# Performance work log

Hardware: AMD Instinct MI355X
Metric: run time of the kernel (lower is better)

The kernel has to match this reference:

```python
import jax, jax.numpy as jnp
import numpy as np

B, N = 4, 2466  # batch, vertex count (Pixel2Mesh stage-3 mesh)
IMG = 224.0


def _vertex_align(feat_maps, pos):
    """Bilinear-style gather of image features at projected vertex locations.
    feat_maps: list of [B,C,S,S]; pos: [B,N,3]. Returns [B,N,sum(C)]."""
    z = pos[..., 2]
    h = jnp.clip(248.0 * (pos[..., 1] / z) + 111.5, 0.0, 223.0)
    w = jnp.clip(248.0 * (pos[..., 0] / (-z)) + 111.5, 0.0, 223.0)
    outs = []
    for f in feat_maps:
        S = f.shape[-1]
        x = h / (IMG / S)
        y = w / (IMG / S)
        x1 = jnp.floor(x).astype(jnp.int32)
        x2 = jnp.minimum(jnp.ceil(x).astype(jnp.int32), S - 1)
        y1 = jnp.floor(y).astype(jnp.int32)
        y2 = jnp.minimum(jnp.ceil(y).astype(jnp.int32), S - 1)
        xi = x.astype(jnp.int32)  # trunc == floor since x >= 0
        yi = y.astype(jnp.int32)

        def gat(fm, xs, ys):  # fm [C,S,S], xs/ys [N] -> [N,C]
            return fm[:, xs, ys].T

        g = jax.vmap(gat)
        w11 = ((x2 - xi) * (y2 - yi)).astype(f.dtype)[..., None]
        w12 = ((x2 - xi) * (yi - y1)).astype(f.dtype)[..., None]
        w21 = ((xi - x1) * (y2 - yi)).astype(f.dtype)[..., None]
        w22 = ((xi - x1) * (yi - y1)).astype(f.dtype)[..., None]
        outs.append(w11 * g(f, x1, y1) + w21 * g(f, x2, y1)
                    + w12 * g(f, x1, y2) + w22 * g(f, x2, y2))
    return jnp.concatenate(outs, axis=-1)


def _graph_conv(x, adj, w0, w1):
    # relu(X @ w0 + A @ (X @ w1))
    return jax.nn.relu(x @ w0 + jnp.einsum('bmn,bnc->bmc', adj, x @ w1))


def _res_graph_conv(x, adj, pw, pb, w00, w01, w10, w11):
    skip = x @ pw + pb
    out = _graph_conv(x, adj, w00, w01)
    out = _graph_conv(out, adj, w10, w11)
    return skip + out


def _forward(conv2_3, conv3_4, conv4_6, conv5_3, vertex_positions, vertex_features,
             vertex_adjacency, lin_w, lin_b,
             r0_pw, r0_pb, r0_w00, r0_w01, r0_w10, r0_w11,
             r1_pw, r1_pb, r1_w00, r1_w01, r1_w10, r1_w11,
             r2_pw, r2_pb, r2_w00, r2_w01, r2_w10, r2_w11,
             gf_w0, gf_w1):
    aligned = _vertex_align([conv2_3, conv3_4, conv4_6, conv5_3], vertex_positions)  # [B,N,3840]
    proj = aligned @ lin_w + lin_b  # [B,N,128]
    x = jnp.concatenate([proj, vertex_features, vertex_positions], axis=-1)  # [B,N,259]
    x = _res_graph_conv(x, vertex_adjacency, r0_pw, r0_pb, r0_w00, r0_w01, r0_w10, r0_w11)
    x = _res_graph_conv(x, vertex_adjacency, r1_pw, r1_pb, r1_w00, r1_w01, r1_w10, r1_w11)
    x = _res_graph_conv(x, vertex_adjacency, r2_pw, r2_pb, r2_w00, r2_w01, r2_w10, r2_w11)
    offset = jnp.tanh(_graph_conv(x, vertex_adjacency, gf_w0, gf_w1))  # [B,N,3]
    return vertex_positions + offset


def setup_inputs() -> dict:
    key = jax.random.key(0)
    ks = jax.random.split(key, 40)
    inp = {
        "conv2_3": jax.random.normal(ks[0], (B, 256, 56, 56), jnp.float32),
        "conv3_4": jax.random.normal(ks[1], (B, 512, 28, 28), jnp.float32),
        "conv4_6": jax.random.normal(ks[2], (B, 1024, 14, 14), jnp.float32),
        "conv5_3": jax.random.normal(ks[3], (B, 2048, 7, 7), jnp.float32),
        "vertex_positions": jax.random.normal(ks[4], (B, N, 3), jnp.float32),
        "vertex_features": jax.random.normal(ks[5], (B, N, 128), jnp.float32),
        # sparse 0/1 adjacency stored dense (the torch module uses dense bmm)
        "vertex_adjacency": (jax.random.uniform(ks[6], (B, N, N)) < 0.003).astype(jnp.float32),
    }

    def u(k, shape, fan):
        b = 1.0 / np.sqrt(fan)
        return jax.random.uniform(k, shape, jnp.float32, -b, b)

    specs = [("lin_w", (3840, 128), 3840), ("lin_b", (128,), 3840)]
    for j, ci in enumerate([259, 128, 128]):
        p = f"r{j}_"
        specs += [(p + "pw", (ci, 128), ci), (p + "pb", (128,), ci),
                  (p + "w00", (ci, 128), ci), (p + "w01", (ci, 128), ci),
                  (p + "w10", (128, 128), 128), (p + "w11", (128, 128), 128)]
    specs += [("gf_w0", (128, 3), 128), ("gf_w1", (128, 3), 128)]
    for i, (name, shape, fan) in enumerate(specs):
        inp[name] = u(ks[7 + i], shape, fan)
    return inp


def reference(conv2_3, conv3_4, conv4_6, conv5_3, vertex_positions, vertex_features,
              vertex_adjacency, lin_w, lin_b,
              r0_pw, r0_pb, r0_w00, r0_w01, r0_w10, r0_w11,
              r1_pw, r1_pb, r1_w00, r1_w01, r1_w10, r1_w11,
              r2_pw, r2_pb, r2_w00, r2_w01, r2_w10, r2_w11,
              gf_w0, gf_w1):
    return _forward(conv2_3, conv3_4, conv4_6, conv5_3, vertex_positions, vertex_features,
                    vertex_adjacency, lin_w, lin_b,
                    r0_pw, r0_pb, r0_w00, r0_w01, r0_w10, r0_w11,
                    r1_pw, r1_pb, r1_w00, r1_w01, r1_w10, r1_w11,
                    r2_pw, r2_pb, r2_w00, r2_w01, r2_w10, r2_w11,
                    gf_w0, gf_w1)
```

## Files before the change

kernel.cpp:

```cpp
#include <hip/hip_runtime.h>
#include <cmath>

#define B_   4
#define N_   2466
#define R_   (B_*N_)
#define ELLW 96

typedef _Float16 f16x8 __attribute__((ext_vector_type(8)));
typedef _Float16 f16x4 __attribute__((ext_vector_type(4)));
typedef __attribute__((ext_vector_type(4))) float f32x4;

__device__ __forceinline__ unsigned short f16_bits(float x) {
  union { _Float16 h; unsigned short u; } c;
  c.h = (_Float16)x;
  return c.u;
}

struct WMats { const float* p[15]; };


__global__ __launch_bounds__(256) void k_pre(
    const float* __restrict__ c2, const float* __restrict__ c3,
    const float* __restrict__ c4, const float* __restrict__ c5,
    unsigned short* __restrict__ t0, unsigned short* __restrict__ t1,
    unsigned short* __restrict__ t2, unsigned short* __restrict__ t3,
    const float* __restrict__ adj, int* __restrict__ cols, int* __restrict__ cnts,
    const float* __restrict__ lin_w,
    unsigned short* __restrict__ whf,
    WMats wm,
    unsigned short* __restrict__ wrf) {
  __shared__ float t[64][66];
  int bid = blockIdx.x;
  int tid = threadIdx.x;
  if (bid < 1584) {
    const float* in; unsigned short* out; int C, P, npb, ncb, rem;
    if (bid < 784)       { in = c2; out = t0; C = 256;  P = 3136; npb = 49; ncb = 4;  rem = bid; }
    else if (bid < 1200) { in = c3; out = t1; C = 512;  P = 784;  npb = 13; ncb = 8;  rem = bid - 784; }
    else if (bid < 1456) { in = c4; out = t2; C = 1024; P = 196;  npb = 4;  ncb = 16; rem = bid - 1200; }
    else                 { in = c5; out = t3; C = 2048; P = 49;   npb = 1;  ncb = 32; rem = bid - 1456; }
    int pb = rem % npb; int tq = rem / npb; int cb = tq % ncb; int b = tq / ncb;
    int c0 = cb * 64, p0 = pb * 64;
    #pragma unroll
    for (int i = 0; i < 8; i++) {
      int e = tid + i * 256;
      int c = e >> 5, f2 = e & 31;
      int p = p0 + f2 * 2;
      float2 v = make_float2(0.f, 0.f);
      const float* src = in + ((size_t)b * C + (c0 + c)) * P + p;
      if (p + 1 < P)      v = *(const float2*)src;
      else if (p < P)     v.x = *src;
      *(float2*)&t[c][f2 * 2] = v;
    }
    __syncthreads();
    int jj = tid & 15, c4i = jj * 4;
    #pragma unroll
    for (int pass = 0; pass < 4; pass++) {
      int pp = pass * 16 + (tid >> 4);
      int px = p0 + pp;
      if (px < P) {
        ushort4 o;
        o.x = f16_bits(t[c4i + 0][pp]);
        o.y = f16_bits(t[c4i + 1][pp]);
        o.z = f16_bits(t[c4i + 2][pp]);
        o.w = f16_bits(t[c4i + 3][pp]);
        *(ushort4*)&out[((size_t)b * P + px) * C + c0 + c4i] = o;
      }
    }
  } else if (bid < 4050) {
    int wave = tid >> 6, lane = tid & 63;
    int row = (bid - 1584) * 4 + wave;
    const float* Ar = adj + (size_t)row * N_;
    int* cp = cols + (size_t)row * ELLW;
    unsigned long long below = (lane == 63) ? 0xFFFFFFFFFFFFFFFFull >> 1
                                            : ((1ull << lane) - 1ull);
    float4 v[10];
    #pragma unroll
    for (int i0 = 0; i0 < 10; i0++) {
      int j0 = i0 * 256 + lane * 4;
      if (j0 + 3 < N_) {
        v[i0] = *(const float4*)&Ar[j0];
      } else {
        v[i0] = make_float4(0.f, 0.f, 0.f, 0.f);
        if (j0     < N_) v[i0].x = Ar[j0];
        if (j0 + 1 < N_) v[i0].y = Ar[j0+1];
        if (j0 + 2 < N_) v[i0].z = Ar[j0+2];
      }
    }
    int base = 0;
    #pragma unroll
    for (int i0 = 0; i0 < 10; i0++) {
      int j0 = i0 * 256 + lane * 4;
      bool nz0 = (j0     < N_) && (v[i0].x != 0.f);
      bool nz1 = (j0 + 1 < N_) && (v[i0].y != 0.f);
      bool nz2 = (j0 + 2 < N_) && (v[i0].z != 0.f);
      bool nz3 = (j0 + 3 < N_) && (v[i0].w != 0.f);
      unsigned long long m0 = __ballot(nz0);
      unsigned long long m1 = __ballot(nz1);
      unsigned long long m2 = __ballot(nz2);
      unsigned long long m3 = __ballot(nz3);
      int pre = __popcll(m0 & below) + __popcll(m1 & below)
              + __popcll(m2 & below) + __popcll(m3 & below);
      int p0 = base + pre;
      int p1 = p0 + (nz0 ? 1 : 0);
      int p2 = p1 + (nz1 ? 1 : 0);
      int p3 = p2 + (nz2 ? 1 : 0);
      if (nz0 && p0 < ELLW) cp[p0] = j0;
      if (nz1 && p1 < ELLW) cp[p1] = j0 + 1;
      if (nz2 && p2 < ELLW) cp[p2] = j0 + 2;
      if (nz3 && p3 < ELLW) cp[p3] = j0 + 3;
      base += __popcll(m0) + __popcll(m1) + __popcll(m2) + __popcll(m3);
    }
    if (lane == 0) cnts[row] = (base > ELLW) ? ELLW : base;
  } else if (bid < 4530) {
    int b = bid - 4050;
    int e0 = (b * 256 + tid) * 4;
    #pragma unroll
    for (int u = 0; u < 4; u++) {
      int e = e0 + u;
      int j = e & 7;
      int lane = (e >> 3) & 63;
      int nt = (e >> 9) & 7;
      int slab = e >> 12;
      int k = slab * 32 + ((lane >> 4) << 3) + j;
      int n = nt * 16 + (lane & 15);
      whf[e] = f16_bits(lin_w[(size_t)k * 128 + n]);
    }
  } else {
    int b = bid - 4530;
    int e0 = (b * 256 + tid) * 4;
    #pragma unroll
    for (int u = 0; u < 4; u++) {
      int e = e0 + u;
      int rb, mat, rem, K;
      if (e < 143360) {
        rb = 0;
        if (e < 110592) { mat = e / 36864; rem = e - mat * 36864; K = 259; }
        else { int tt = e - 110592; mat = 3 + tt / 16384; rem = tt & 16383; K = 128; }
      } else {
        int tt = e - 143360;
        rb = 1 + tt / 81920;
        int r2 = tt % 81920;
        mat = r2 / 16384; rem = r2 & 16383; K = 128;
      }
      int j = rem & 7, lane = (rem >> 3) & 63, nt = (rem >> 9) & 7, slab = rem >> 12;
      int k = slab * 32 + ((lane >> 4) << 3) + j;
      int n = nt * 16 + (lane & 15);
      float x = (k < K) ? wm.p[rb * 5 + mat][(size_t)k * 128 + n] : 0.f;
      wrf[e] = f16_bits(x);
    }
  }
}

__global__ __launch_bounds__(256) void k_align_mfma(
    const unsigned short* __restrict__ tr0, const unsigned short* __restrict__ tr1,
    const unsigned short* __restrict__ tr2, const unsigned short* __restrict__ tr3,
    const float* __restrict__ pos,
    const unsigned short* __restrict__ whf,
    unsigned short* __restrict__ part, int kchunk) {
  int tid  = threadIdx.x;
  int wave = tid >> 6, lane = tid & 63;
  int q    = lane >> 4, l15 = lane & 15;
  int m0   = blockIdx.x * 128;
  int s    = blockIdx.y;

  int zero[2][4]; int base[2][4];
  #pragma unroll
  for (int u = 0; u < 2; u++) {
    int mrow = m0 + (wave * 2 + u) * 16 + l15;
    int rowc = (mrow < R_) ? mrow : 0;
    int b = rowc / N_;
    float px = pos[rowc*3+0], py = pos[rowc*3+1], pz = pos[rowc*3+2];
    float hh = fminf(fmaxf(248.f*(py/pz)    + 111.5f, 0.f), 223.f);
    float wc = fminf(fmaxf(248.f*(px/(-pz)) + 111.5f, 0.f), 223.f);
    const int Sarr[4] = {56, 28, 14, 7};
    const int Carr[4] = {256, 512, 1024, 2048};
    #pragma unroll
    for (int sc = 0; sc < 4; sc++) {
      int S = Sarr[sc], C = Carr[sc];
      float dv = 224.f / (float)S;
      float x = hh / dv, y = wc / dv;
      int x1 = (int)floorf(x), y1 = (int)floorf(y);
      int x2 = min((int)ceilf(x), S - 1), y2 = min((int)ceilf(y), S - 1);
      int w = (x2 - x1) * (y2 - y1);
      zero[u][sc] = (mrow >= R_) || (w == 0);
      base[u][sc] = (b * S * S + x1 * S + y1) * C;
    }
  }

  f32x4 acc[2][8];
  #pragma unroll
  for (int u = 0; u < 2; u++)
    #pragma unroll
    for (int nt = 0; nt < 8; nt++) acc[u][nt] = (f32x4){0.f, 0.f, 0.f, 0.f};

  const f16x8* BH = (const f16x8*)whf;

  int kbeg = s * kchunk, kend = kbeg + kchunk;
  #pragma unroll 1
  for (int k0 = kbeg; k0 < kend; k0 += 32) {
    const unsigned short* tr; int off, sI;
    if (k0 < 256)       { tr = tr0; off = 0;    sI = 0; }
    else if (k0 < 768)  { tr = tr1; off = 256;  sI = 1; }
    else if (k0 < 1792) { tr = tr2; off = 768;  sI = 2; }
    else                { tr = tr3; off = 1792; sI = 3; }

    f16x8 af[2];
    #pragma unroll
    for (int u = 0; u < 2; u++) {
      af[u] = *(const f16x8*)(tr + base[u][sI] + (k0 - off) + q * 8);
      if (zero[u][sI]) af[u] = (f16x8)(_Float16)0;
    }

    int slab = k0 >> 5;
    f16x8 Bh[8];
    #pragma unroll
    for (int nt = 0; nt < 8; nt++)
      Bh[nt] = BH[(size_t)(slab * 8 + nt) * 64 + lane];
    #pragma unroll
    for (int nt = 0; nt < 8; nt++) {
      acc[0][nt] = __builtin_amdgcn_mfma_f32_16x16x32_f16(af[0], Bh[nt], acc[0][nt], 0, 0, 0);
      acc[1][nt] = __builtin_amdgcn_mfma_f32_16x16x32_f16(af[1], Bh[nt], acc[1][nt], 0, 0, 0);
    }
  }

  #pragma unroll
  for (int u = 0; u < 2; u++)
    #pragma unroll
    for (int nt = 0; nt < 8; nt++)
      #pragma unroll
      for (int r = 0; r < 4; r++) {
        int row = m0 + (wave * 2 + u) * 16 + q * 4 + r;
        if (row < R_)
          part[((size_t)s * R_ + row) * 128 + nt * 16 + l15] = f16_bits(acc[u][nt][r]);
      }
}

__global__ __launch_bounds__(256) void k_reduce(
    const unsigned short* __restrict__ part, const float* __restrict__ lin_b,
    const float* __restrict__ vf, const float* __restrict__ pos,
    unsigned short* __restrict__ xcat, int nsplit) {
  int grp = threadIdx.x >> 5, ln = threadIdx.x & 31;
  int row = blockIdx.x * 8 + grp;
  float4 acc = ((const float4*)lin_b)[ln];
  const f16x4* p4 = (const f16x4*)part;
  for (int s = 0; s < nsplit; s++) {
    f16x4 pv = p4[((size_t)s * R_ + row) * 32 + ln];
    acc.x += (float)pv[0]; acc.y += (float)pv[1];
    acc.z += (float)pv[2]; acc.w += (float)pv[3];
  }
  ushort4* xr = (ushort4*)(xcat + (size_t)row * 288);
  ushort4 o;
  o.x = f16_bits(acc.x); o.y = f16_bits(acc.y);
  o.z = f16_bits(acc.z); o.w = f16_bits(acc.w);
  xr[ln] = o;
  float4 vv = ((const float4*)vf)[(size_t)row * 32 + ln];
  o.x = f16_bits(vv.x); o.y = f16_bits(vv.y);
  o.z = f16_bits(vv.z); o.w = f16_bits(vv.w);
  xr[32 + ln] = o;
  if (ln < 8) {
    ushort4 z = make_ushort4(0, 0, 0, 0);
    if (ln == 0) {
      z.x = f16_bits(pos[(size_t)row * 3 + 0]);
      z.y = f16_bits(pos[(size_t)row * 3 + 1]);
      z.z = f16_bits(pos[(size_t)row * 3 + 2]);
    }
    xr[64 + ln] = z;
  }
}

template<int SLABS>
__global__ __launch_bounds__(256) void k_gemm_mfma(
    const unsigned short* __restrict__ X, int ldx,
    const unsigned short* __restrict__ wf,
    int matStride, const float* __restrict__ pb,
    unsigned short* __restrict__ o0, unsigned short* __restrict__ o1,
    unsigned short* __restrict__ o2) {
  int tid = threadIdx.x;
  int wave = tid >> 6, lane = tid & 63;
  int q = lane >> 4, l15 = lane & 15;
  int which = blockIdx.y;
  int m0 = blockIdx.x * 64;
  int mrow = m0 + wave * 16 + l15;
  int rowc = (mrow < R_) ? mrow : (R_ - 1);
  const unsigned short* xrow = X + (size_t)rowc * ldx + q * 8;

  const f16x8* BH = (const f16x8*)(wf + (size_t)which * matStride);

  f32x4 acc[8];
  #pragma unroll
  for (int nt = 0; nt < 8; nt++) acc[nt] = (f32x4){0.f, 0.f, 0.f, 0.f};

  #pragma unroll 1
  for (int slab = 0; slab < SLABS; slab++) {
    f16x8 af = *(const f16x8*)(xrow + slab * 32);
    f16x8 Bh[8];
    #pragma unroll
    for (int nt = 0; nt < 8; nt++)
      Bh[nt] = BH[(size_t)(slab * 8 + nt) * 64 + lane];
    #pragma unroll
    for (int nt = 0; nt < 8; nt++)
      acc[nt] = __builtin_amdgcn_mfma_f32_16x16x32_f16(af, Bh[nt], acc[nt], 0, 0, 0);
  }

  unsigned short* out = (which == 0) ? o0 : (which == 1) ? o1 : o2;
  #pragma unroll
  for (int nt = 0; nt < 8; nt++) {
    int col = nt * 16 + l15;
    float bias = (pb != nullptr && which == 2) ? pb[col] : 0.f;
    #pragma unroll
    for (int r = 0; r < 4; r++) {
      int row = m0 + wave * 16 + q * 4 + r;
      if (row < R_) out[(size_t)row * 128 + col] = f16_bits(acc[nt][r] + bias);
    }
  }
}

template<int NW>
__global__ __launch_bounds__(256) void k_fuse(
    const unsigned short* __restrict__ s_in,
    const unsigned short* __restrict__ t_in,
    const unsigned short* __restrict__ skip_in,
    const int* __restrict__ cols, const int* __restrict__ cnts,
    const unsigned short* __restrict__ wf, const float* __restrict__ pb,
    unsigned short* __restrict__ o0, unsigned short* __restrict__ o1,
    unsigned short* __restrict__ o2) {
  __shared__ unsigned short hsm[32][136];
  int tid = threadIdx.x;
  int r0 = blockIdx.x * 32;

  {
    int grp = tid >> 5, ln = tid & 31;
    const f16x4* s4 = (const f16x4*)s_in;
    const f16x4* t4 = (const f16x4*)t_in;
    #pragma unroll 1
    for (int rr = 0; rr < 4; rr++) {
      int lrow = grp * 4 + rr;
      int row = r0 + lrow;
      int rowc = (row < R_) ? row : (R_ - 1);
      int b = rowc / N_;
      size_t tbase = (size_t)b * N_;
      const int* cp = cols + (size_t)rowc * ELLW;
      int4 ci0 = *(const int4*)cp;
      int4 ci1 = *(const int4*)(cp + 4);
      int4 ci2 = *(const int4*)(cp + 8);
      int cnt = cnts[rowc];
      f16x4 sv = s4[(size_t)rowc*32 + ln];
      float4 acc = make_float4((float)sv[0], (float)sv[1], (float)sv[2], (float)sv[3]);
      int idx[12] = {ci0.x, ci0.y, ci0.z, ci0.w, ci1.x, ci1.y, ci1.z, ci1.w,
                     ci2.x, ci2.y, ci2.z, ci2.w};
      f16x4 g[12];
      #pragma unroll
      for (int i = 0; i < 12; i++) {
        int c = idx[i];
        c = (c >= 0 && c < N_) ? c : 0;
        g[i] = t4[(tbase + c)*32 + ln];
      }
      #pragma unroll
      for (int i = 0; i < 12; i++) {
        if (i < cnt) {
          acc.x += (float)g[i][0]; acc.y += (float)g[i][1];
          acc.z += (float)g[i][2]; acc.w += (float)g[i][3];
        }
      }
      for (int i = 12; i < cnt; i++) {
        f16x4 v = t4[(tbase + cp[i])*32 + ln];
        acc.x += (float)v[0]; acc.y += (float)v[1];
        acc.z += (float)v[2]; acc.w += (float)v[3];
      }
      acc.x = fmaxf(acc.x, 0.f); acc.y = fmaxf(acc.y, 0.f);
      acc.z = fmaxf(acc.z, 0.f); acc.w = fmaxf(acc.w, 0.f);
      if (skip_in) {
        f16x4 sk = ((const f16x4*)skip_in)[(size_t)rowc*32 + ln];
        acc.x += (float)sk[0]; acc.y += (float)sk[1];
        acc.z += (float)sk[2]; acc.w += (float)sk[3];
      }
      ushort4 o;
      o.x = f16_bits(acc.x); o.y = f16_bits(acc.y);
      o.z = f16_bits(acc.z); o.w = f16_bits(acc.w);
      *(ushort4*)&hsm[lrow][ln * 4] = o;
    }
  }
  __syncthreads();

  int wave = tid >> 6, lane = tid & 63;
  int q = lane >> 4, l15 = lane & 15;
  int mt = wave & 1, nh = wave >> 1;
  const unsigned short* xrow = &hsm[mt * 16 + l15][q * 8];

  #pragma unroll 1
  for (int which = 0; which < NW; which++) {
    const f16x8* BH = (const f16x8*)(wf + (size_t)which * 16384);
    f32x4 acc[4];
    #pragma unroll
    for (int t2 = 0; t2 < 4; t2++) acc[t2] = (f32x4){0.f, 0.f, 0.f, 0.f};
    #pragma unroll
    for (int slab = 0; slab < 4; slab++) {
      f16x8 af = *(const f16x8*)(xrow + slab * 32);
      f16x8 Bh[4];
      #pragma unroll
      for (int t2 = 0; t2 < 4; t2++)
        Bh[t2] = BH[(size_t)(slab * 8 + nh * 4 + t2) * 64 + lane];
      #pragma unroll
      for (int t2 = 0; t2 < 4; t2++)
        acc[t2] = __builtin_amdgcn_mfma_f32_16x16x32_f16(af, Bh[t2], acc[t2], 0, 0, 0);
    }
    unsigned short* out = (which == 0) ? o0 : (which == 1) ? o1 : o2;
    #pragma unroll
    for (int t2 = 0; t2 < 4; t2++) {
      int col = (nh * 4 + t2) * 16 + l15;
      float bias = (pb != nullptr && which == 2) ? pb[col] : 0.f;
      #pragma unroll
      for (int r = 0; r < 4; r++) {
        int row = r0 + mt * 16 + q * 4 + r;
        if (row < R_) out[(size_t)row * 128 + col] = f16_bits(acc[t2][r] + bias);
      }
    }
  }
}

__global__ __launch_bounds__(256) void k_spmm(
    const unsigned short* __restrict__ sb, const unsigned short* __restrict__ tb,
    const int* __restrict__ cols, const int* __restrict__ cnts,
    const unsigned short* __restrict__ skipb, unsigned short* __restrict__ outb,
    const float* __restrict__ gw0, const float* __restrict__ gw1,
    unsigned short* __restrict__ gsb, unsigned short* __restrict__ gtb, int fuse_gf) {
  int tid = threadIdx.x;
  int grp = tid >> 5, ln = tid & 31;
  int row = blockIdx.x * 8 + grp;
  int b = row / N_;
  size_t tbase = (size_t)b * N_;
  const f16x4* sb4 = (const f16x4*)sb;
  const f16x4* tb4 = (const f16x4*)tb;
  const int* cp = cols + (size_t)row * ELLW;
  int4 ci0 = *(const int4*)cp;
  int4 ci1 = *(const int4*)(cp + 4);
  int4 ci2 = *(const int4*)(cp + 8);
  int cnt = cnts[row];
  f16x4 sv = sb4[(size_t)row*32 + ln];
  float4 acc = make_float4((float)sv[0], (float)sv[1], (float)sv[2], (float)sv[3]);
  int idx[12] = {ci0.x, ci0.y, ci0.z, ci0.w, ci1.x, ci1.y, ci1.z, ci1.w,
                 ci2.x, ci2.y, ci2.z, ci2.w};
  f16x4 g[12];
  #pragma unroll
  for (int i = 0; i < 12; i++) {
    int c = idx[i];
    c = (c >= 0 && c < N_) ? c : 0;
    g[i] = tb4[(tbase + c)*32 + ln];
  }
  #pragma unroll
  for (int i = 0; i < 12; i++) {
    if (i < cnt) {
      acc.x += (float)g[i][0]; acc.y += (float)g[i][1];
      acc.z += (float)g[i][2]; acc.w += (float)g[i][3];
    }
  }
  for (int i = 12; i < cnt; i++) {
    f16x4 v = tb4[(tbase + cp[i])*32 + ln];
    acc.x += (float)v[0]; acc.y += (float)v[1];
    acc.z += (float)v[2]; acc.w += (float)v[3];
  }
  acc.x = fmaxf(acc.x, 0.f); acc.y = fmaxf(acc.y, 0.f);
  acc.z = fmaxf(acc.z, 0.f); acc.w = fmaxf(acc.w, 0.f);
  if (skipb) {
    f16x4 sk = ((const f16x4*)skipb)[(size_t)row*32 + ln];
    acc.x += (float)sk[0]; acc.y += (float)sk[1];
    acc.z += (float)sk[2]; acc.w += (float)sk[3];
  }
  if (!fuse_gf) {
    ushort4 o;
    o.x = f16_bits(acc.x); o.y = f16_bits(acc.y);
    o.z = f16_bits(acc.z); o.w = f16_bits(acc.w);
    ((ushort4*)outb)[(size_t)row*32 + ln] = o;
    return;
  }
  float av[4] = {acc.x, acc.y, acc.z, acc.w};
  int j0 = ln * 4;
  float p0 = 0.f, p1 = 0.f, p2 = 0.f, q0 = 0.f, q1 = 0.f, q2 = 0.f;
  #pragma unroll
  for (int u = 0; u < 4; u++) {
    int j = j0 + u;
    p0 += av[u] * gw0[j*3+0]; p1 += av[u] * gw0[j*3+1]; p2 += av[u] * gw0[j*3+2];
    q0 += av[u] * gw1[j*3+0]; q1 += av[u] * gw1[j*3+1]; q2 += av[u] * gw1[j*3+2];
  }
  #pragma unroll
  for (int off = 16; off >= 1; off >>= 1) {
    p0 += __shfl_xor(p0, off); p1 += __shfl_xor(p1, off); p2 += __shfl_xor(p2, off);
    q0 += __shfl_xor(q0, off); q1 += __shfl_xor(q1, off); q2 += __shfl_xor(q2, off);
  }
  if (ln == 0) {
    gsb[(size_t)row*128 + 0] = f16_bits(p0);
    gsb[(size_t)row*128 + 1] = f16_bits(p1);
    gsb[(size_t)row*128 + 2] = f16_bits(p2);
    gtb[(size_t)row*128 + 0] = f16_bits(q0);
    gtb[(size_t)row*128 + 1] = f16_bits(q1);
    gtb[(size_t)row*128 + 2] = f16_bits(q2);
  }
}

__global__ __launch_bounds__(256) void k_gf_final(
    const unsigned short* __restrict__ sb, const unsigned short* __restrict__ tb,
    const int* __restrict__ cols, const int* __restrict__ cnts,
    const float* __restrict__ pos, float* __restrict__ out) {
  int wave = threadIdx.x >> 6, lane = threadIdx.x & 63;
  int row = blockIdx.x * 4 + wave;
  if (lane >= 3) return;
  int b = row / N_;
  size_t tbase = (size_t)b * N_;
  const int* cp = cols + (size_t)row * ELLW;
  int4 ci0 = *(const int4*)cp;
  int4 ci1 = *(const int4*)(cp + 4);
  int4 ci2 = *(const int4*)(cp + 8);
  int cnt = cnts[row];
  union { unsigned short u; _Float16 h; } cv;
  cv.u = sb[(size_t)row*128 + lane];
  float acc = (float)cv.h;
  int idx[12] = {ci0.x, ci0.y, ci0.z, ci0.w, ci1.x, ci1.y, ci1.z, ci1.w,
                 ci2.x, ci2.y, ci2.z, ci2.w};
  float g[12];
  #pragma unroll
  for (int i = 0; i < 12; i++) {
    int c = idx[i];
    c = (c >= 0 && c < N_) ? c : 0;
    cv.u = tb[(tbase + c)*128 + lane];
    g[i] = (float)cv.h;
  }
  #pragma unroll
  for (int i = 0; i < 12; i++)
    if (i < cnt) acc += g[i];
  for (int i = 12; i < cnt; i++) {
    cv.u = tb[(tbase + cp[i])*128 + lane];
    acc += (float)cv.h;
  }
  float v = tanhf(fmaxf(acc, 0.f));
  out[(size_t)row*3 + lane] = pos[(size_t)row*3 + lane] + v;
}

extern "C" void kernel_launch(void* const* d_in, const int* in_sizes, int n_in,
                              void* d_out, int out_size, void* d_ws, size_t ws_size,
                              hipStream_t stream) {
  const float* conv2_3 = (const float*)d_in[0];
  const float* conv3_4 = (const float*)d_in[1];
  const float* conv4_6 = (const float*)d_in[2];
  const float* conv5_3 = (const float*)d_in[3];
  const float* pos     = (const float*)d_in[4];
  const float* vf      = (const float*)d_in[5];
  const float* adj     = (const float*)d_in[6];
  const float* lin_w   = (const float*)d_in[7];
  const float* lin_b   = (const float*)d_in[8];
  const float* r_pb[3]  = {(const float*)d_in[10], (const float*)d_in[16], (const float*)d_in[22]};
  const float* gf_w0 = (const float*)d_in[27];
  const float* gf_w1 = (const float*)d_in[28];
  float* out = (float*)d_out;

  const size_t ROWF    = (size_t)R_ * 128;
  const size_t XCATE   = (size_t)R_ * 288;
  const size_t LINW_E  = 491520;
  const size_t RESW_E  = 307200;

  unsigned short* trh0 = (unsigned short*)d_ws;
  unsigned short* trh1 = trh0 + (size_t)4*256*3136;
  unsigned short* trh2 = trh1 + (size_t)4*512*784;
  unsigned short* trh3 = trh2 + (size_t)4*1024*196;
  int*   ell_cnt  = (int*)(trh3 + (size_t)4*2048*49);
  int*   ell_cols = ell_cnt + R_;
  unsigned short* whf = (unsigned short*)(ell_cols + (size_t)R_*ELLW);
  unsigned short* wrf = whf + LINW_E;
  unsigned short* part = wrf + RESW_E + 512;

  size_t fixed_h = 6021120 + 2*(size_t)R_*(ELLW+1) + LINW_E + RESW_E + 512;
  size_t need8 = (fixed_h + (size_t)8*ROWF + XCATE + 8*ROWF + 1024) * 2;
  int nsplit = (ws_size >= need8) ? 8 : 4;
  int kchunk = 3840 / nsplit;

  unsigned short* xcat = part + (size_t)nsplit * ROWF;
  unsigned short* sb   = xcat + XCATE;
  unsigned short* tb   = sb   + ROWF;
  unsigned short* sb2  = tb   + ROWF;
  unsigned short* tb2  = sb2  + ROWF;
  unsigned short* skA  = tb2  + ROWF;
  unsigned short* skB  = skA  + ROWF;
  unsigned short* gsb  = skB  + ROWF;
  unsigned short* gtb  = gsb  + ROWF;

  WMats wm;
  for (int rb = 0; rb < 3; rb++) {
    wm.p[rb*5 + 0] = (const float*)d_in[11 + 6*rb];
    wm.p[rb*5 + 1] = (const float*)d_in[12 + 6*rb];
    wm.p[rb*5 + 2] = (const float*)d_in[9  + 6*rb];
    wm.p[rb*5 + 3] = (const float*)d_in[13 + 6*rb];
    wm.p[rb*5 + 4] = (const float*)d_in[14 + 6*rb];
  }

  const int NFB = (R_ + 31) / 32;

  k_pre<<<4830, 256, 0, stream>>>(conv2_3, conv3_4, conv4_6, conv5_3,
                                  trh0, trh1, trh2, trh3,
                                  adj, ell_cols, ell_cnt,
                                  lin_w, whf, wm, wrf);

  k_align_mfma<<<dim3(78, nsplit), 256, 0, stream>>>(trh0, trh1, trh2, trh3, pos,
                                                     whf, part, kchunk);

  k_reduce<<<1233, 256, 0, stream>>>(part, lin_b, vf, pos, xcat, nsplit);

  k_gemm_mfma<9><<<dim3(155, 3), 256, 0, stream>>>(
      xcat, 288, wrf + 0, 36864, r_pb[0], sb, tb, skA);

  k_fuse<2><<<NFB, 256, 0, stream>>>(sb, tb, nullptr, ell_cols, ell_cnt,
                                     wrf + 110592, nullptr, sb2, tb2, nullptr);

  k_fuse<3><<<NFB, 256, 0, stream>>>(sb2, tb2, skA, ell_cols, ell_cnt,
                                     wrf + 143360, r_pb[1], sb, tb, skB);

  k_fuse<2><<<NFB, 256, 0, stream>>>(sb, tb, nullptr, ell_cols, ell_cnt,
                                     wrf + 192512, nullptr, sb2, tb2, nullptr);

  k_fuse<3><<<NFB, 256, 0, stream>>>(sb2, tb2, skB, ell_cols, ell_cnt,
                                     wrf + 225280, r_pb[2], sb, tb, skA);

  k_fuse<2><<<NFB, 256, 0, stream>>>(sb, tb, nullptr, ell_cols, ell_cnt,
                                     wrf + 274432, nullptr, sb2, tb2, nullptr);

  k_spmm<<<1233, 256, 0, stream>>>(sb2, tb2, ell_cols, ell_cnt, skA, nullptr,
                                   gf_w0, gf_w1, gsb, gtb, 1);

  k_gf_final<<<2466, 256, 0, stream>>>(gsb, gtb, ell_cols, ell_cnt, pos, out);
}
```

Measured before the change: 380.1 us.

## Split vertex feature gather into separate kernel writing MFMA-ready A tiles

```diff
diff --git a/kernel.cpp b/kernel.cpp
--- a/kernel.cpp
+++ b/kernel.cpp
@@ -151,10 +151,54 @@
   }
 }
 
-__global__ __launch_bounds__(256) void k_align_mfma(
+__global__ __launch_bounds__(256) void k_gather(
     const unsigned short* __restrict__ tr0, const unsigned short* __restrict__ tr1,
     const unsigned short* __restrict__ tr2, const unsigned short* __restrict__ tr3,
-    const float* __restrict__ pos,
+    const float* __restrict__ pos, unsigned short* __restrict__ xg) {
+  int grp = threadIdx.x >> 5, ln = threadIdx.x & 31;
+  int row = blockIdx.x * 8 + grp;
+  int mtile = row >> 4, l15 = row & 15;
+  int zero[4]; int base[4];
+  if (row < R_) {
+    int b = row / N_;
+    float px = pos[row*3+0], py = pos[row*3+1], pz = pos[row*3+2];
+    float hh = fminf(fmaxf(248.f*(py/pz)    + 111.5f, 0.f), 223.f);
+    float wc = fminf(fmaxf(248.f*(px/(-pz)) + 111.5f, 0.f), 223.f);
+    const int Sarr[4] = {56, 28, 14, 7};
+    const int Carr[4] = {256, 512, 1024, 2048};
+    #pragma unroll
+    for (int sc = 0; sc < 4; sc++) {
+      int S = Sarr[sc], C = Carr[sc];
+      float dv = 224.f / (float)S;
+      float x = hh / dv, y = wc / dv;
+      int x1 = (int)floorf(x), y1 = (int)floorf(y);
+      int x2 = min((int)ceilf(x), S - 1), y2 = min((int)ceilf(y), S - 1);
+      int w = (x2 - x1) * (y2 - y1);
+      zero[sc] = (w == 0);
+      base[sc] = (b * S * S + x1 * S + y1) * C;
+    }
+  } else {
+    zero[0] = zero[1] = zero[2] = zero[3] = 1;
+    base[0] = base[1] = base[2] = base[3] = 0;
+  }
+  #pragma unroll
+  for (int i = 0; i < 15; i++) {
+    int k0 = (i * 32 + ln) * 8;
+    const unsigned short* tr; int off, sI;
+    if (k0 < 256)       { tr = tr0; off = 0;    sI = 0; }
+    else if (k0 < 768)  { tr = tr1; off = 256;  sI = 1; }
+    else if (k0 < 1792) { tr = tr2; off = 768;  sI = 2; }
+    else                { tr = tr3; off = 1792; sI = 3; }
+    f16x8 v;
+    if (zero[sI]) v = (f16x8)(_Float16)0;
+    else          v = *(const f16x8*)(tr + base[sI] + (k0 - off));
+    int slab = k0 >> 5, q = (k0 >> 3) & 3;
+    *(f16x8*)&xg[(((size_t)mtile * 120 + slab) * 64 + q * 16 + l15) * 8] = v;
+  }
+}
+
+__global__ __launch_bounds__(256) void k_align_mfma(
+    const unsigned short* __restrict__ xg,
     const unsigned short* __restrict__ whf,
     unsigned short* __restrict__ part, int kchunk) {
   int tid  = threadIdx.x;
@@ -162,30 +206,7 @@
   int q    = lane >> 4, l15 = lane & 15;
   int m0   = blockIdx.x * 128;
   int s    = blockIdx.y;
-
-  int zero[2][4]; int base[2][4];
-  #pragma unroll
-  for (int u = 0; u < 2; u++) {
-    int mrow = m0 + (wave * 2 + u) * 16 + l15;
-    int rowc = (mrow < R_) ? mrow : 0;
-    int b = rowc / N_;
-    float px = pos[rowc*3+0], py = pos[rowc*3+1], pz = pos[rowc*3+2];
-    float hh = fminf(fmaxf(248.f*(py/pz)    + 111.5f, 0.f), 223.f);
-    float wc = fminf(fmaxf(248.f*(px/(-pz)) + 111.5f, 0.f), 223.f);
-    const int Sarr[4] = {56, 28, 14, 7};
-    const int Carr[4] = {256, 512, 1024, 2048};
-    #pragma unroll
-    for (int sc = 0; sc < 4; sc++) {
-      int S = Sarr[sc], C = Carr[sc];
-      float dv = 224.f / (float)S;
-      float x = hh / dv, y = wc / dv;
-      int x1 = (int)floorf(x), y1 = (int)floorf(y);
-      int x2 = min((int)ceilf(x), S - 1), y2 = min((int)ceilf(y), S - 1);
-      int w = (x2 - x1) * (y2 - y1);
-      zero[u][sc] = (mrow >= R_) || (w == 0);
-      base[u][sc] = (b * S * S + x1 * S + y1) * C;
-    }
-  }
+  int mt0  = blockIdx.x * 8 + wave * 2;
 
   f32x4 acc[2][8];
   #pragma unroll
@@ -194,32 +215,22 @@
     for (int nt = 0; nt < 8; nt++) acc[u][nt] = (f32x4){0.f, 0.f, 0.f, 0.f};
 
   const f16x8* BH = (const f16x8*)whf;
+  const f16x8* XG = (const f16x8*)xg;
 
   int kbeg = s * kchunk, kend = kbeg + kchunk;
   #pragma unroll 1
   for (int k0 = kbeg; k0 < kend; k0 += 32) {
-    const unsigned short* tr; int off, sI;
-    if (k0 < 256)       { tr = tr0; off = 0;    sI = 0; }
-    else if (k0 < 768)  { tr = tr1; off = 256;  sI = 1; }
-    else if (k0 < 1792) { tr = tr2; off = 768;  sI = 2; }
-    else                { tr = tr3; off = 1792; sI = 3; }
-
-    f16x8 af[2];
-    #pragma unroll
-    for (int u = 0; u < 2; u++) {
-      af[u] = *(const f16x8*)(tr + base[u][sI] + (k0 - off) + q * 8);
-      if (zero[u][sI]) af[u] = (f16x8)(_Float16)0;
-    }
-
     int slab = k0 >> 5;
+    f16x8 af0 = XG[((size_t)(mt0 + 0) * 120 + slab) * 64 + lane];
+    f16x8 af1 = XG[((size_t)(mt0 + 1) * 120 + slab) * 64 + lane];
     f16x8 Bh[8];
     #pragma unroll
     for (int nt = 0; nt < 8; nt++)
       Bh[nt] = BH[(size_t)(slab * 8 + nt) * 64 + lane];
     #pragma unroll
     for (int nt = 0; nt < 8; nt++) {
-      acc[0][nt] = __builtin_amdgcn_mfma_f32_16x16x32_f16(af[0], Bh[nt], acc[0][nt], 0, 0, 0);
-      acc[1][nt] = __builtin_amdgcn_mfma_f32_16x16x32_f16(af[1], Bh[nt], acc[1][nt], 0, 0, 0);
+      acc[0][nt] = __builtin_amdgcn_mfma_f32_16x16x32_f16(af0, Bh[nt], acc[0][nt], 0, 0, 0);
+      acc[1][nt] = __builtin_amdgcn_mfma_f32_16x16x32_f16(af1, Bh[nt], acc[1][nt], 0, 0, 0);
     }
   }
 
@@ -556,6 +567,7 @@
   const size_t XCATE   = (size_t)R_ * 288;
   const size_t LINW_E  = 491520;
   const size_t RESW_E  = 307200;
+  const size_t XG_E    = (size_t)624 * 120 * 512;
 
   unsigned short* trh0 = (unsigned short*)d_ws;
   unsigned short* trh1 = trh0 + (size_t)4*256*3136;
@@ -568,7 +580,7 @@
   unsigned short* part = wrf + RESW_E + 512;
 
   size_t fixed_h = 6021120 + 2*(size_t)R_*(ELLW+1) + LINW_E + RESW_E + 512;
-  size_t need8 = (fixed_h + (size_t)8*ROWF + XCATE + 8*ROWF + 1024) * 2;
+  size_t need8 = (fixed_h + (size_t)8*ROWF + XCATE + 8*ROWF + XG_E + 1024) * 2;
   int nsplit = (ws_size >= need8) ? 8 : 4;
   int kchunk = 3840 / nsplit;
 
@@ -581,6 +593,7 @@
   unsigned short* skB  = skA  + ROWF;
   unsigned short* gsb  = skB  + ROWF;
   unsigned short* gtb  = gsb  + ROWF;
+  unsigned short* xg   = gtb  + ROWF;
 
   WMats wm;
   for (int rb = 0; rb < 3; rb++) {
@@ -598,8 +611,9 @@
                                   adj, ell_cols, ell_cnt,
                                   lin_w, whf, wm, wrf);
 
-  k_align_mfma<<<dim3(78, nsplit), 256, 0, stream>>>(trh0, trh1, trh2, trh3, pos,
-                                                     whf, part, kchunk);
+  k_gather<<<1248, 256, 0, stream>>>(trh0, trh1, trh2, trh3, pos, xg);
+
+  k_align_mfma<<<dim3(78, nsplit), 256, 0, stream>>>(xg, whf, part, kchunk);
 
   k_reduce<<<1233, 256, 0, stream>>>(part, lin_b, vf, pos, xcat, nsplit);
 
```

New measurement: 419.7 us. +10.4%, slower.

## Split adjacency ELL build across four waves per row and shrink GEMM/fuse tiles

Applied to the files above, without the earlier changes.

```diff
diff --git a/kernel.cpp b/kernel.cpp
--- a/kernel.cpp
+++ b/kernel.cpp
@@ -66,41 +66,57 @@
         *(ushort4*)&out[((size_t)b * P + px) * C + c0 + c4i] = o;
       }
     }
-  } else if (bid < 4050) {
-    int wave = tid >> 6, lane = tid & 63;
-    int row = (bid - 1584) * 4 + wave;
+  } else if (bid < 11448) {
+    int row = bid - 1584;
+    int wv = tid >> 6, lane = tid & 63;
     const float* Ar = adj + (size_t)row * N_;
     int* cp = cols + (size_t)row * ELLW;
     unsigned long long below = (lane == 63) ? 0xFFFFFFFFFFFFFFFFull >> 1
                                             : ((1ull << lane) - 1ull);
-    float4 v[10];
-    #pragma unroll
-    for (int i0 = 0; i0 < 10; i0++) {
-      int j0 = i0 * 256 + lane * 4;
-      if (j0 + 3 < N_) {
-        v[i0] = *(const float4*)&Ar[j0];
+    int jbeg = wv * 640;
+    int jend = (jbeg + 640 < N_) ? jbeg + 640 : N_;
+    unsigned long long m[3][4];
+    int cnt = 0;
+    #pragma unroll
+    for (int i = 0; i < 3; i++) {
+      int j0 = jbeg + i * 256 + lane * 4;
+      float4 v = make_float4(0.f, 0.f, 0.f, 0.f);
+      if (j0 + 3 < jend) {
+        v = *(const float4*)&Ar[j0];
       } else {
-        v[i0] = make_float4(0.f, 0.f, 0.f, 0.f);
-        if (j0     < N_) v[i0].x = Ar[j0];
-        if (j0 + 1 < N_) v[i0].y = Ar[j0+1];
-        if (j0 + 2 < N_) v[i0].z = Ar[j0+2];
-      }
-    }
+        if (j0     < jend) v.x = Ar[j0];
+        if (j0 + 1 < jend) v.y = Ar[j0+1];
+        if (j0 + 2 < jend) v.z = Ar[j0+2];
+      }
+      m[i][0] = __ballot((j0     < jend) && (v.x != 0.f));
+      m[i][1] = __ballot((j0 + 1 < jend) && (v.y != 0.f));
+      m[i][2] = __ballot((j0 + 2 < jend) && (v.z != 0.f));
+      m[i][3] = __ballot((j0 + 3 < jend) && (v.w != 0.f));
+      cnt += __popcll(m[i][0]) + __popcll(m[i][1])
+           + __popcll(m[i][2]) + __popcll(m[i][3]);
+    }
+    int* sc = (int*)&t[0][0];
+    if (lane == 0) sc[wv] = cnt;
+    __syncthreads();
     int base = 0;
     #pragma unroll
-    for (int i0 = 0; i0 < 10; i0++) {
-      int j0 = i0 * 256 + lane * 4;
-      bool nz0 = (j0     < N_) && (v[i0].x != 0.f);
-      bool nz1 = (j0 + 1 < N_) && (v[i0].y != 0.f);
-      bool nz2 = (j0 + 2 < N_) && (v[i0].z != 0.f);
-      bool nz3 = (j0 + 3 < N_) && (v[i0].w != 0.f);
-      unsigned long long m0 = __ballot(nz0);
-      unsigned long long m1 = __ballot(nz1);
-      unsigned long long m2 = __ballot(nz2);
-      unsigned long long m3 = __ballot(nz3);
+    for (int w2 = 0; w2 < 4; w2++) {
+      int c = sc[w2];
+      if (w2 < wv) base += c;
+    }
+    int tot = sc[0] + sc[1] + sc[2] + sc[3];
+    int run = base;
+    #pragma unroll
+    for (int i = 0; i < 3; i++) {
+      int j0 = jbeg + i * 256 + lane * 4;
+      unsigned long long m0 = m[i][0], m1 = m[i][1], m2 = m[i][2], m3 = m[i][3];
       int pre = __popcll(m0 & below) + __popcll(m1 & below)
               + __popcll(m2 & below) + __popcll(m3 & below);
-      int p0 = base + pre;
+      bool nz0 = (m0 >> lane) & 1ull;
+      bool nz1 = (m1 >> lane) & 1ull;
+      bool nz2 = (m2 >> lane) & 1ull;
+      bool nz3 = (m3 >> lane) & 1ull;
+      int p0 = run + pre;
       int p1 = p0 + (nz0 ? 1 : 0);
       int p2 = p1 + (nz1 ? 1 : 0);
       int p3 = p2 + (nz2 ? 1 : 0);
@@ -108,11 +124,11 @@
       if (nz1 && p1 < ELLW) cp[p1] = j0 + 1;
       if (nz2 && p2 < ELLW) cp[p2] = j0 + 2;
       if (nz3 && p3 < ELLW) cp[p3] = j0 + 3;
-      base += __popcll(m0) + __popcll(m1) + __popcll(m2) + __popcll(m3);
-    }
-    if (lane == 0) cnts[row] = (base > ELLW) ? ELLW : base;
-  } else if (bid < 4530) {
-    int b = bid - 4050;
+      run += __popcll(m0) + __popcll(m1) + __popcll(m2) + __popcll(m3);
+    }
+    if (wv == 3 && lane == 0) cnts[row] = (tot > ELLW) ? ELLW : tot;
+  } else if (bid < 11928) {
+    int b = bid - 11448;
     int e0 = (b * 256 + tid) * 4;
     #pragma unroll
     for (int u = 0; u < 4; u++) {
@@ -126,7 +142,7 @@
       whf[e] = f16_bits(lin_w[(size_t)k * 128 + n]);
     }
   } else {
-    int b = bid - 4530;
+    int b = bid - 11928;
     int e0 = (b * 256 + tid) * 4;
     #pragma unroll
     for (int u = 0; u < 4; u++) {
@@ -279,38 +295,39 @@
   int wave = tid >> 6, lane = tid & 63;
   int q = lane >> 4, l15 = lane & 15;
   int which = blockIdx.y;
-  int m0 = blockIdx.x * 64;
-  int mrow = m0 + wave * 16 + l15;
+  int m0 = blockIdx.x * 32;
+  int mt = wave & 1, nh = wave >> 1;
+  int mrow = m0 + mt * 16 + l15;
   int rowc = (mrow < R_) ? mrow : (R_ - 1);
   const unsigned short* xrow = X + (size_t)rowc * ldx + q * 8;
 
   const f16x8* BH = (const f16x8*)(wf + (size_t)which * matStride);
 
-  f32x4 acc[8];
-  #pragma unroll
-  for (int nt = 0; nt < 8; nt++) acc[nt] = (f32x4){0.f, 0.f, 0.f, 0.f};
+  f32x4 acc[4];
+  #pragma unroll
+  for (int t2 = 0; t2 < 4; t2++) acc[t2] = (f32x4){0.f, 0.f, 0.f, 0.f};
 
   #pragma unroll 1
   for (int slab = 0; slab < SLABS; slab++) {
     f16x8 af = *(const f16x8*)(xrow + slab * 32);
-    f16x8 Bh[8];
-    #pragma unroll
-    for (int nt = 0; nt < 8; nt++)
-      Bh[nt] = BH[(size_t)(slab * 8 + nt) * 64 + lane];
-    #pragma unroll
-    for (int nt = 0; nt < 8; nt++)
-      acc[nt] = __builtin_amdgcn_mfma_f32_16x16x32_f16(af, Bh[nt], acc[nt], 0, 0, 0);
+    f16x8 Bh[4];
+    #pragma unroll
+    for (int t2 = 0; t2 < 4; t2++)
+      Bh[t2] = BH[(size_t)(slab * 8 + nh * 4 + t2) * 64 + lane];
+    #pragma unroll
+    for (int t2 = 0; t2 < 4; t2++)
+      acc[t2] = __builtin_amdgcn_mfma_f32_16x16x32_f16(af, Bh[t2], acc[t2], 0, 0, 0);
   }
 
   unsigned short* out = (which == 0) ? o0 : (which == 1) ? o1 : o2;
   #pragma unroll
-  for (int nt = 0; nt < 8; nt++) {
-    int col = nt * 16 + l15;
+  for (int t2 = 0; t2 < 4; t2++) {
+    int col = (nh * 4 + t2) * 16 + l15;
     float bias = (pb != nullptr && which == 2) ? pb[col] : 0.f;
     #pragma unroll
     for (int r = 0; r < 4; r++) {
-      int row = m0 + wave * 16 + q * 4 + r;
-      if (row < R_) out[(size_t)row * 128 + col] = f16_bits(acc[nt][r] + bias);
+      int row = m0 + mt * 16 + q * 4 + r;
+      if (row < R_) out[(size_t)row * 128 + col] = f16_bits(acc[t2][r] + bias);
     }
   }
 }
@@ -324,17 +341,17 @@
     const unsigned short* __restrict__ wf, const float* __restrict__ pb,
     unsigned short* __restrict__ o0, unsigned short* __restrict__ o1,
     unsigned short* __restrict__ o2) {
-  __shared__ unsigned short hsm[32][136];
+  __shared__ unsigned short hsm[16][136];
   int tid = threadIdx.x;
-  int r0 = blockIdx.x * 32;
+  int r0 = blockIdx.x * 16;
 
   {
     int grp = tid >> 5, ln = tid & 31;
     const f16x4* s4 = (const f16x4*)s_in;
     const f16x4* t4 = (const f16x4*)t_in;
     #pragma unroll 1
-    for (int rr = 0; rr < 4; rr++) {
-      int lrow = grp * 4 + rr;
+    for (int rr = 0; rr < 2; rr++) {
+      int lrow = grp * 2 + rr;
       int row = r0 + lrow;
       int rowc = (row < R_) ? row : (R_ - 1);
       int b = rowc / N_;
@@ -384,34 +401,33 @@
 
   int wave = tid >> 6, lane = tid & 63;
   int q = lane >> 4, l15 = lane & 15;
-  int mt = wave & 1, nh = wave >> 1;
-  const unsigned short* xrow = &hsm[mt * 16 + l15][q * 8];
+  const unsigned short* xrow = &hsm[l15][q * 8];
 
   #pragma unroll 1
   for (int which = 0; which < NW; which++) {
     const f16x8* BH = (const f16x8*)(wf + (size_t)which * 16384);
-    f32x4 acc[4];
-    #pragma unroll
-    for (int t2 = 0; t2 < 4; t2++) acc[t2] = (f32x4){0.f, 0.f, 0.f, 0.f};
+    f32x4 acc[2];
+    #pragma unroll
+    for (int t2 = 0; t2 < 2; t2++) acc[t2] = (f32x4){0.f, 0.f, 0.f, 0.f};
     #pragma unroll
     for (int slab = 0; slab < 4; slab++) {
       f16x8 af = *(const f16x8*)(xrow + slab * 32);
-      f16x8 Bh[4];
+      f16x8 Bh[2];
       #pragma unroll
-      for (int t2 = 0; t2 < 4; t2++)
-        Bh[t2] = BH[(size_t)(slab * 8 + nh * 4 + t2) * 64 + lane];
+      for (int t2 = 0; t2 < 2; t2++)
+        Bh[t2] = BH[(size_t)(slab * 8 + wave * 2 + t2) * 64 + lane];
       #pragma unroll
-      for (int t2 = 0; t2 < 4; t2++)
+      for (int t2 = 0; t2 < 2; t2++)
         acc[t2] = __builtin_amdgcn_mfma_f32_16x16x32_f16(af, Bh[t2], acc[t2], 0, 0, 0);
     }
     unsigned short* out = (which == 0) ? o0 : (which == 1) ? o1 : o2;
     #pragma unroll
-    for (int t2 = 0; t2 < 4; t2++) {
-      int col = (nh * 4 + t2) * 16 + l15;
+    for (int t2 = 0; t2 < 2; t2++) {
+      int col = (wave * 2 + t2) * 16 + l15;
       float bias = (pb != nullptr && which == 2) ? pb[col] : 0.f;
       #pragma unroll
       for (int r = 0; r < 4; r++) {
-        int row = r0 + mt * 16 + q * 4 + r;
+        int row = r0 + q * 4 + r;
         if (row < R_) out[(size_t)row * 128 + col] = f16_bits(acc[t2][r] + bias);
       }
     }
@@ -591,19 +607,20 @@
     wm.p[rb*5 + 4] = (const float*)d_in[14 + 6*rb];
   }
 
-  const int NFB = (R_ + 31) / 32;
-
-  k_pre<<<4830, 256, 0, stream>>>(conv2_3, conv3_4, conv4_6, conv5_3,
-                                  trh0, trh1, trh2, trh3,
-                                  adj, ell_cols, ell_cnt,
-                                  lin_w, whf, wm, wrf);
+  const int NFB = (R_ + 15) / 16;
+  const int NGB = (R_ + 31) / 32;
+
+  k_pre<<<12228, 256, 0, stream>>>(conv2_3, conv3_4, conv4_6, conv5_3,
+                                   trh0, trh1, trh2, trh3,
+                                   adj, ell_cols, ell_cnt,
+                                   lin_w, whf, wm, wrf);
 
   k_align_mfma<<<dim3(78, nsplit), 256, 0, stream>>>(trh0, trh1, trh2, trh3, pos,
                                                      whf, part, kchunk);
 
   k_reduce<<<1233, 256, 0, stream>>>(part, lin_b, vf, pos, xcat, nsplit);
 
-  k_gemm_mfma<9><<<dim3(155, 3), 256, 0, stream>>>(
+  k_gemm_mfma<9><<<dim3(NGB, 3), 256, 0, stream>>>(
       xcat, 288, wrf + 0, 36864, r_pb[0], sb, tb, skA);
 
   k_fuse<2><<<NFB, 256, 0, stream>>>(sb, tb, nullptr, ell_cols, ell_cnt,
```

Result: faster. 349.2 us (-8.1%).
